# Kernel tuning notes

Hardware: AMD Instinct MI355X
Metric: run time of the kernel (lower is better)

Reference implementation:

```python
import jax, jax.numpy as jnp
import numpy as np

N = 40000   # nodes
E = 150000  # edges (before self-loops)
G = 128     # graphs in batch
V = 20000   # vocab
D = 512     # embedding/hidden dim
H = 4       # heads (layers 0,1)
C = 128     # per-head channels (H*C = D)


def setup_inputs() -> dict:
    key = jax.random.key(0)
    ks = jax.random.split(key, 64)
    n = lambda i, shp, s=0.05: jax.random.normal(ks[i], shp, dtype=jnp.float32) * s
    inp = {}
    inp['node_ids'] = jax.random.randint(ks[0], (N,), 0, V, dtype=jnp.int32)
    inp['edge_index'] = jax.random.randint(ks[1], (2, E), 0, N, dtype=jnp.int32)
    inp['batch'] = jnp.sort(jax.random.randint(ks[2], (N,), 0, G, dtype=jnp.int32))
    inp['emb'] = n(3, (V, D), 0.02)
    # GAT layer 0: D -> H x C, concat
    inp['W0'] = n(4, (D, H * C)); inp['as0'] = n(5, (H, C)); inp['ad0'] = n(6, (H, C)); inp['b0'] = n(7, (D,), 0.01)
    # GAT layer 1: D -> H x C, concat
    inp['W1'] = n(8, (D, H * C)); inp['as1'] = n(9, (H, C)); inp['ad1'] = n(10, (H, C)); inp['b1'] = n(11, (D,), 0.01)
    inp['W2'] = n(12, (D, D)); inp['as2'] = n(13, (1, D)); inp['ad2'] = n(14, (1, D)); inp['b2'] = n(15, (D,), 0.01)
    # danger head
    inp['dW1'] = n(16, (D, D)); inp['db1'] = n(17, (D,), 0.01)
    inp['dg1'] = 1.0 + n(18, (D,), 0.02); inp['dbt1'] = n(19, (D,), 0.02)
    inp['drm1'] = n(20, (D,), 0.02); inp['drv1'] = jax.random.uniform(ks[21], (D,)) + 0.5
    inp['dW2'] = n(22, (D, D // 2)); inp['db2'] = n(23, (D // 2,), 0.01)
    inp['dg2'] = 1.0 + n(24, (D // 2,), 0.02); inp['dbt2'] = n(25, (D // 2,), 0.02)
    inp['drm2'] = n(26, (D // 2,), 0.02); inp['drv2'] = jax.random.uniform(ks[27], (D // 2,)) + 0.5
    inp['dW3'] = n(28, (D // 2, 1)); inp['db3'] = n(29, (1,), 0.01)
    # synergy head
    inp['sW1'] = n(30, (D, D)); inp['sb1'] = n(31, (D,), 0.01)
    inp['sg1'] = 1.0 + n(32, (D,), 0.02); inp['sbt1'] = n(33, (D,), 0.02)
    inp['srm1'] = n(34, (D,), 0.02); inp['srv1'] = jax.random.uniform(ks[35], (D,)) + 0.5
    inp['sW2'] = n(36, (D, D // 2)); inp['sb2'] = n(37, (D // 2,), 0.01)
    inp['sg2'] = 1.0 + n(38, (D // 2,), 0.02); inp['sbt2'] = n(39, (D // 2,), 0.02)
    inp['srm2'] = n(40, (D // 2,), 0.02); inp['srv2'] = jax.random.uniform(ks[41], (D // 2,)) + 0.5
    inp['sW3'] = n(42, (D // 2, 1)); inp['sb3'] = n(43, (1,), 0.01)
    return inp


def _gat(x, W, a_src, a_dst, bias, src, dst, heads, ch, concat):
    # PyG GATConv (eval): linear, per-head additive attention, softmax over
    # incoming edges per destination node, scatter-add aggregate.
    n_nodes = x.shape[0]
    h = (x @ W).reshape(n_nodes, heads, ch)              # [N,H,C]
    e_s = jnp.sum(h * a_src, axis=-1)                    # [N,H]
    e_d = jnp.sum(h * a_dst, axis=-1)                    # [N,H]
    e = jax.nn.leaky_relu(e_s[src] + e_d[dst], 0.2)      # [E,H]
    m = jax.ops.segment_max(e, dst, num_segments=n_nodes)
    m = jnp.where(jnp.isfinite(m), m, 0.0)
    p = jnp.exp(e - m[dst])
    s = jax.ops.segment_sum(p, dst, num_segments=n_nodes)
    alpha = p / (s[dst] + 1e-16)                         # [E,H]
    out = jax.ops.segment_sum(h[src] * alpha[:, :, None], dst, num_segments=n_nodes)
    out = out.reshape(n_nodes, heads * ch) if concat else out.mean(axis=1)
    return out + bias


def _bn(x, g, b, rm, rv):
    return (x - rm) * jax.lax.rsqrt(rv + 1e-5) * g + b


def _head(p, W1, b1, g1, bt1, rm1, rv1, W2, b2, g2, bt2, rm2, rv2, W3, b3):
    z = jax.nn.relu(_bn(p @ W1 + b1, g1, bt1, rm1, rv1))
    z = jax.nn.relu(_bn(z @ W2 + b2, g2, bt2, rm2, rv2))
    return jax.nn.sigmoid(z @ W3 + b3)


def reference(node_ids, edge_index, batch, emb, W0, as0, ad0, b0, W1, as1, ad1, b1, W2, as2, ad2, b2, dW1, db1, dg1, dbt1, drm1, drv1, dW2, db2, dg2, dbt2, drm2, drv2, dW3, db3, sW1, sb1, sg1, sbt1, srm1, srv1, sW2, sb2, sg2, sbt2, srm2, srv2, sW3, sb3):
    loops = jnp.arange(N, dtype=edge_index.dtype)
    src = jnp.concatenate([edge_index[0], loops])
    dst = jnp.concatenate([edge_index[1], loops])
    x = emb[node_ids]                                    # [N,D]
    # layer 0 (no residual)
    x = jax.nn.relu(_gat(x, W0, as0, ad0, b0, src, dst, H, C, True))
    # layer 1 (+residual)
    x = x + jax.nn.relu(_gat(x, W1, as1, ad1, b1, src, dst, H, C, True))
    # layer 2 (+residual)
    x = x + jax.nn.relu(_gat(x, W2, as2, ad2, b2, src, dst, 1, D, False))
    # global mean pool per graph
    sums = jax.ops.segment_sum(x, batch, num_segments=G)
    cnt = jax.ops.segment_sum(jnp.ones((N,), x.dtype), batch, num_segments=G)
    pooled = sums / jnp.maximum(cnt, 1.0)[:, None]       # [G,D]
    danger = _head(pooled, dW1, db1, dg1, dbt1, drm1, drv1, dW2, db2, dg2, dbt2, drm2, drv2, dW3, db3)
    synergy = _head(pooled, sW1, sb1, sg1, sbt1, srm1, srv1, sW2, sb2, sg2, sbt2, srm2, srv2, sW3, sb3)
    return danger, synergy
```

## Files before the change

### kernel.cpp

```cpp
#include <hip/hip_runtime.h>
#include <hip/hip_bf16.h>
#include <stdint.h>

#define NN 40000
#define EE 150000
#define ET 190000
#define GG 128
#define DD 512
#define MP 40064
#define SCAN_B 157
#define PS 16
#define GNB 1252
#define GNBF 1248

typedef __hip_bfloat16 bf16;
typedef __attribute__((ext_vector_type(8))) short s16x8;
typedef __attribute__((ext_vector_type(4))) float f32v4;

__device__ __forceinline__ float b2f(bf16 v) { return __bfloat162float(v); }
__device__ __forceinline__ bf16  f2b(float v) { return __float2bfloat16(v); }
__device__ __forceinline__ unsigned f2bu(float v) {
    bf16 b = __float2bfloat16(v);
    return (unsigned)*(unsigned short*)&b;
}
__device__ __forceinline__ float lo16(unsigned u) { return __uint_as_float(u << 16); }
__device__ __forceinline__ float hi16(unsigned u) { return __uint_as_float(u & 0xffff0000u); }
__device__ __forceinline__ float s2f(short s) {
    return __uint_as_float(((unsigned)(unsigned short)s) << 16);
}

__global__ __launch_bounds__(256) void k_gather_emb(const int* __restrict__ ids,
                                                    const float4* __restrict__ emb4,
                                                    bf16* __restrict__ xb) {
    int t = blockIdx.x * 256 + threadIdx.x;
    int n = t >> 7, c = t & 127;
    if (n >= NN) return;
    int id = ids[n];
    float4 v = emb4[(size_t)id * 128 + c];
    ushort4 u;
    u.x = (unsigned short)f2bu(v.x); u.y = (unsigned short)f2bu(v.y);
    u.z = (unsigned short)f2bu(v.z); u.w = (unsigned short)f2bu(v.w);
    *(ushort4*)(xb + (size_t)n * DD + c * 4) = u;
}

__global__ __launch_bounds__(256) void k_w2bf_t3(const float* __restrict__ W0,
                                                 const float* __restrict__ W1,
                                                 const float* __restrict__ W2,
                                                 bf16* __restrict__ Wt0,
                                                 bf16* __restrict__ Wt1,
                                                 bf16* __restrict__ Wt2) {
    const float* W; bf16* Wt;
    if (blockIdx.z == 0)      { W = W0; Wt = Wt0; }
    else if (blockIdx.z == 1) { W = W1; Wt = Wt1; }
    else                      { W = W2; Wt = Wt2; }
    __shared__ float tile[64][65];
    int tid = threadIdx.x;
    int n0 = blockIdx.x * 64, k0 = blockIdx.y * 64;
    int rr = tid >> 4, cc = (tid & 15) * 4;
    #pragma unroll
    for (int i = 0; i < 4; i++) {
        int k = k0 + i * 16 + rr;
        float4 v = *(const float4*)(W + (size_t)k * DD + n0 + cc);
        tile[cc + 0][i * 16 + rr] = v.x;
        tile[cc + 1][i * 16 + rr] = v.y;
        tile[cc + 2][i * 16 + rr] = v.z;
        tile[cc + 3][i * 16 + rr] = v.w;
    }
    __syncthreads();
    #pragma unroll
    for (int i = 0; i < 4; i++) {
        int nl = i * 16 + rr;
        ushort4 o;
        o.x = (unsigned short)f2bu(tile[nl][cc + 0]);
        o.y = (unsigned short)f2bu(tile[nl][cc + 1]);
        o.z = (unsigned short)f2bu(tile[nl][cc + 2]);
        o.w = (unsigned short)f2bu(tile[nl][cc + 3]);
        *(ushort4*)(Wt + (size_t)(n0 + nl) * DD + k0 + cc) = o;
    }
}

template <int H>
__global__ __launch_bounds__(256) void k_gemm_mfma(const bf16* __restrict__ A,
                                                   const bf16* __restrict__ Bt,
                                                   bf16* __restrict__ C,
                                                   const float* __restrict__ a_s,
                                                   const float* __restrict__ a_d,
                                                   float* __restrict__ es,
                                                   float* __restrict__ ed) {
    constexpr int K = DD, N = DD;
    constexpr int LSTR = 72;
    __shared__ bf16 smem[2 * 128 * LSTR];
    bf16* lA = smem;
    bf16* lB = smem + 128 * LSTR;
    int tid = threadIdx.x, lane = tid & 63, quad = lane >> 4, l16 = lane & 15;
    int w = tid >> 6;

    int bid = blockIdx.x, mt, nt;
    if (bid >= GNBF) { mt = MP / 128 - 1; nt = bid - GNBF; }
    else { nt = (bid & 31) >> 3; mt = (bid >> 5) * 8 + (bid & 7); }
    int m0 = mt * 128, n0 = nt * 128;
    int wm = (w & 1) * 64, wn = (w >> 1) * 64;

    int sdst[4]; const bf16 *pA[4], *pB[4];
    #pragma unroll
    for (int r = 0; r < 4; r++) {
        int q = r * 256 + tid;
        int row = q >> 3, c = q & 7;
        sdst[r] = row * LSTR + c * 8;
        pA[r] = A + (size_t)(m0 + row) * K + c * 8;
        pB[r] = Bt + (size_t)(n0 + row) * K + c * 8;
    }
    int aoff[2][4], boff[2][4];
    #pragma unroll
    for (int kk = 0; kk < 2; kk++)
        #pragma unroll
        for (int i = 0; i < 4; i++) {
            aoff[kk][i] = (wm + i * 16 + l16) * LSTR + (kk * 4 + quad) * 8;
            boff[kk][i] = (wn + i * 16 + l16) * LSTR + (kk * 4 + quad) * 8;
        }

    f32v4 zero = 0;
    f32v4 acc[4][4];
    #pragma unroll
    for (int i = 0; i < 4; i++)
        #pragma unroll
        for (int j = 0; j < 4; j++) acc[i][j] = zero;

    for (int k0 = 0; k0 < K; k0 += 64) {
        __syncthreads();
        #pragma unroll
        for (int r = 0; r < 4; r++) {
            *(s16x8*)(lA + sdst[r]) = *(const s16x8*)(pA[r] + k0);
            *(s16x8*)(lB + sdst[r]) = *(const s16x8*)(pB[r] + k0);
        }
        __syncthreads();
        #pragma unroll
        for (int kk = 0; kk < 2; kk++) {
            s16x8 a[4], b[4];
            #pragma unroll
            for (int i = 0; i < 4; i++) a[i] = *(const s16x8*)(lA + aoff[kk][i]);
            #pragma unroll
            for (int j = 0; j < 4; j++) b[j] = *(const s16x8*)(lB + boff[kk][j]);
            #pragma unroll
            for (int i = 0; i < 4; i++)
                #pragma unroll
                for (int j = 0; j < 4; j++)
                    acc[i][j] = __builtin_amdgcn_mfma_f32_16x16x32_bf16(a[i], b[j], acc[i][j], 0, 0, 0);
        }
    }

    float* asl = (float*)(smem + 8192);
    float* adl = asl + 128;
    __syncthreads();
    if (tid < 128) asl[tid] = a_s[n0 + tid];
    else           adl[tid - 128] = a_d[n0 + tid - 128];

    constexpr int ESTR = 136;
    bf16* ebuf = smem;
    int lrB = (w & 1) * 16 + quad * 4;
    int lr = tid >> 3, cc8 = (tid & 7) * 16;
    int grow = m0 + (lr >> 4) * 64 + (lr & 15);
    int headIdx = (H == 4) ? nt : 0;
    #pragma unroll
    for (int i = 0; i < 4; i++) {
        __syncthreads();
        #pragma unroll
        for (int j = 0; j < 4; j++) {
            int col = wn + j * 16 + l16;
            #pragma unroll
            for (int r = 0; r < 4; r++)
                ebuf[(lrB + r) * ESTR + col] = f2b(acc[i][j][r]);
        }
        __syncthreads();
        s16x8 v0 = *(s16x8*)(ebuf + lr * ESTR + cc8);
        s16x8 v1 = *(s16x8*)(ebuf + lr * ESTR + cc8 + 8);
        float ses = 0.f, sed = 0.f;
        #pragma unroll
        for (int k = 0; k < 8; k++) {
            float x = s2f(v0[k]);
            ses += x * asl[cc8 + k];
            sed += x * adl[cc8 + k];
        }
        #pragma unroll
        for (int k = 0; k < 8; k++) {
            float x = s2f(v1[k]);
            ses += x * asl[cc8 + 8 + k];
            sed += x * adl[cc8 + 8 + k];
        }
        #pragma unroll
        for (int off = 1; off < 8; off <<= 1) {
            ses += __shfl_xor(ses, off, 64);
            sed += __shfl_xor(sed, off, 64);
        }
        int row = grow + i * 16;
        if ((tid & 7) == 0) {
            atomicAdd(es + (size_t)row * H + headIdx, ses);
            atomicAdd(ed + (size_t)row * H + headIdx, sed);
        }
        size_t o = (size_t)row * N + n0 + cc8;
        *(s16x8*)(C + o) = v0;
        *(s16x8*)(C + o + 8) = v1;
    }
}

__global__ __launch_bounds__(256) void k_count_deg(const int* __restrict__ edst,
                                                   int* __restrict__ deg) {
    int e = blockIdx.x * 256 + threadIdx.x;
    if (e >= ET) return;
    int dst = (e < EE) ? edst[e] : (e - EE);
    atomicAdd(&deg[dst], 1);
}

__global__ __launch_bounds__(256) void k_scan_local(const int* __restrict__ deg,
                                                    int* __restrict__ offs,
                                                    int* __restrict__ bsum) {
    __shared__ int buf[256];
    int i = blockIdx.x * 256 + threadIdx.x;
    int v = (i < NN) ? deg[i] : 0;
    buf[threadIdx.x] = v;
    __syncthreads();
    #pragma unroll
    for (int off = 1; off < 256; off <<= 1) {
        int t = (threadIdx.x >= (unsigned)off) ? buf[threadIdx.x - off] : 0;
        __syncthreads();
        buf[threadIdx.x] += t;
        __syncthreads();
    }
    if (i < NN) offs[i] = buf[threadIdx.x] - v;
    if (threadIdx.x == 255) bsum[blockIdx.x] = buf[255];
}

__global__ __launch_bounds__(256) void k_scan_add2(int* __restrict__ offs,
                                                   const int* __restrict__ bsum) {
    __shared__ int buf[256];
    __shared__ int s_off;
    int v = (threadIdx.x < SCAN_B) ? bsum[threadIdx.x] : 0;
    buf[threadIdx.x] = v;
    __syncthreads();
    #pragma unroll
    for (int off = 1; off < 256; off <<= 1) {
        int t = (threadIdx.x >= (unsigned)off) ? buf[threadIdx.x - off] : 0;
        __syncthreads();
        buf[threadIdx.x] += t;
        __syncthreads();
    }
    if (threadIdx.x == blockIdx.x) s_off = buf[threadIdx.x] - v;
    __syncthreads();
    int i = blockIdx.x * 256 + threadIdx.x;
    if (i < NN) offs[i] += s_off;
    if (i == 0) offs[NN] = ET;
}

__global__ __launch_bounds__(256) void k_fill_csr(const int* __restrict__ esrc,
                                                  const int* __restrict__ edst,
                                                  const int* __restrict__ offsets,
                                                  int* __restrict__ cursor,
                                                  int* __restrict__ csr_src) {
    int e = blockIdx.x * 256 + threadIdx.x;
    if (e >= ET) return;
    int dst, src;
    if (e < EE) { dst = edst[e]; src = esrc[e]; }
    else        { dst = e - EE;  src = e - EE; }
    int slot = offsets[dst] + atomicAdd(&cursor[dst], 1);
    csr_src[slot] = src;
}

template <int H, bool RES>
__global__ __launch_bounds__(256) void k_gat_aggregate(const bf16* __restrict__ h,
                                                       const float* __restrict__ es,
                                                       const float* __restrict__ ed,
                                                       const int* __restrict__ offsets,
                                                       const int* __restrict__ csr_src,
                                                       const float* __restrict__ bias,
                                                       bf16* __restrict__ xb) {
    __shared__ int   s_src[8][32];
    __shared__ float s_a[8][32 * H];
    __shared__ int   s_deg[8];
    int tid = threadIdx.x, w = tid >> 6, lane = tid & 63;
    int half = lane >> 5, el = lane & 31;
    int nb = blockIdx.x * 8;
    {
        int ln = w * 2 + half;
        int node = nb + ln;
        int beg = offsets[node];
        int deg = offsets[node + 1] - beg;
        if (deg > 32) deg = 32;
        if (el == 0) s_deg[ln] = deg;
        float edl[H];
        #pragma unroll
        for (int hh = 0; hh < H; hh++) edl[hh] = ed[node * H + hh];
        float e_h[H];
        #pragma unroll
        for (int hh = 0; hh < H; hh++) e_h[hh] = -1e30f;
        if (el < deg) {
            int src = csr_src[beg + el];
            s_src[ln][el] = src;
            if (H == 4) {
                float4 e4 = *(const float4*)(es + (size_t)src * 4);
                float t4[4] = {e4.x, e4.y, e4.z, e4.w};
                #pragma unroll
                for (int hh = 0; hh < 4; hh++) {
                    float e = t4[hh] + edl[hh];
                    e_h[hh] = e > 0.f ? e : 0.2f * e;
                }
            } else {
                float e = es[src] + edl[0];
                e_h[0] = e > 0.f ? e : 0.2f * e;
            }
        }
        float m[H];
        #pragma unroll
        for (int hh = 0; hh < H; hh++) m[hh] = e_h[hh];
        #pragma unroll
        for (int off = 16; off; off >>= 1)
            #pragma unroll
            for (int hh = 0; hh < H; hh++) m[hh] = fmaxf(m[hh], __shfl_xor(m[hh], off, 64));
        float p[H], sum[H];
        #pragma unroll
        for (int hh = 0; hh < H; hh++) {
            p[hh] = (el < deg) ? __expf(e_h[hh] - m[hh]) : 0.f;
            sum[hh] = p[hh];
        }
        #pragma unroll
        for (int off = 16; off; off >>= 1)
            #pragma unroll
            for (int hh = 0; hh < H; hh++) sum[hh] += __shfl_xor(sum[hh], off, 64);
        if (el < deg)
            #pragma unroll
            for (int hh = 0; hh < H; hh++) s_a[ln][el * H + hh] = p[hh] / (sum[hh] + 1e-16f);
    }
    __syncthreads();

    int dbase = lane * 8;
    int hd = (H == 4) ? (lane >> 4) : 0;
    float4 bi0 = *(const float4*)(bias + dbase);
    float4 bi1 = *(const float4*)(bias + dbase + 4);
    #pragma unroll
    for (int t = 0; t < 2; t++) {
        int nn = w * 2 + t;
        int deg = s_deg[nn];
        float acc[8] = {};
        for (int i = 0; i < deg; i++) {
            uint4 u = *(const uint4*)(h + (size_t)s_src[nn][i] * DD + dbase);
            float a = s_a[nn][i * H + hd];
            acc[0] += a * lo16(u.x); acc[1] += a * hi16(u.x);
            acc[2] += a * lo16(u.y); acc[3] += a * hi16(u.y);
            acc[4] += a * lo16(u.z); acc[5] += a * hi16(u.z);
            acc[6] += a * lo16(u.w); acc[7] += a * hi16(u.w);
        }
        float v[8];
        v[0] = acc[0] + bi0.x; v[1] = acc[1] + bi0.y;
        v[2] = acc[2] + bi0.z; v[3] = acc[3] + bi0.w;
        v[4] = acc[4] + bi1.x; v[5] = acc[5] + bi1.y;
        v[6] = acc[6] + bi1.z; v[7] = acc[7] + bi1.w;
        #pragma unroll
        for (int k = 0; k < 8; k++) v[k] = fmaxf(v[k], 0.f);
        size_t base = (size_t)(nb + nn) * DD + dbase;
        if (RES) {
            uint4 u = *(const uint4*)(xb + base);
            v[0] += lo16(u.x); v[1] += hi16(u.x);
            v[2] += lo16(u.y); v[3] += hi16(u.y);
            v[4] += lo16(u.z); v[5] += hi16(u.z);
            v[6] += lo16(u.w); v[7] += hi16(u.w);
        }
        uint4 o;
        o.x = f2bu(v[0]) | (f2bu(v[1]) << 16);
        o.y = f2bu(v[2]) | (f2bu(v[3]) << 16);
        o.z = f2bu(v[4]) | (f2bu(v[5]) << 16);
        o.w = f2bu(v[6]) | (f2bu(v[7]) << 16);
        *(uint4*)(xb + base) = o;
    }
}

__global__ __launch_bounds__(256) void k_pool_part(const int* __restrict__ batch,
                                                   const bf16* __restrict__ xb,
                                                   float* __restrict__ psum,
                                                   int* __restrict__ cnt) {
    int g = blockIdx.x, s = blockIdx.y;
    __shared__ int s_lo, s_hi;
    if (threadIdx.x == 0) {
        int lo = 0, hi = NN;
        while (lo < hi) { int mid = (lo + hi) >> 1; if (batch[mid] < g) lo = mid + 1; else hi = mid; }
        s_lo = lo;
        lo = 0; hi = NN;
        while (lo < hi) { int mid = (lo + hi) >> 1; if (batch[mid] < g + 1) lo = mid + 1; else hi = mid; }
        s_hi = lo;
    }
    __syncthreads();
    int lo = s_lo, hi = s_hi, len = hi - lo;
    int na = lo + (int)(((long)len * s) / PS);
    int nb = lo + (int)(((long)len * (s + 1)) / PS);
    int d0 = threadIdx.x * 2;
    float a0 = 0.f, a1 = 0.f;
    for (int n = na; n < nb; n++) {
        unsigned u = *(const unsigned*)(xb + (size_t)n * DD + d0);
        a0 += lo16(u);
        a1 += hi16(u);
    }
    size_t o = ((size_t)s * GG + g) * DD + d0;
    psum[o]     = a0;
    psum[o + 1] = a1;
    if (s == 0 && threadIdx.x == 0) cnt[g] = len;
}

__global__ __launch_bounds__(256) void k_pool_div(const float* __restrict__ psum,
                                                  const int* __restrict__ cnt,
                                                  float* __restrict__ pooled) {
    int idx = blockIdx.x * 256 + threadIdx.x;
    int g = idx >> 9;
    float s = 0.f;
    #pragma unroll
    for (int seg = 0; seg < PS; seg++) s += psum[(size_t)seg * GG * DD + idx];
    pooled[idx] = s / fmaxf((float)cnt[g], 1.f);
}

template <int Din, int Dout>
__global__ __launch_bounds__(256) void k_head_layer2(const float* __restrict__ inD,
                                                     const float* __restrict__ inS,
                                                     const float* __restrict__ Wd, const float* __restrict__ bd,
                                                     const float* __restrict__ gd, const float* __restrict__ btd,
                                                     const float* __restrict__ rmd, const float* __restrict__ rvd,
                                                     const float* __restrict__ Ws, const float* __restrict__ bs_,
                                                     const float* __restrict__ gs, const float* __restrict__ bts,
                                                     const float* __restrict__ rms, const float* __restrict__ rvs,
                                                     float* __restrict__ outD,
                                                     float* __restrict__ outS) {
    const float *in, *W, *b, *ga, *bt, *rm, *rv; float* out;
    if (blockIdx.z == 0) { in = inD; W = Wd; b = bd; ga = gd; bt = btd; rm = rmd; rv = rvd; out = outD; }
    else                 { in = inS; W = Ws; b = bs_; ga = gs; bt = bts; rm = rms; rv = rvs; out = outS; }
    int g = blockIdx.y;
    int tid = threadIdx.x;
    int j = blockIdx.x * 64 + (tid & 63);
    int ks = tid >> 6;
    __shared__ float s_in[Din];
    __shared__ float s_red[256];
    for (int k = tid; k < Din; k += 256) s_in[k] = in[(size_t)g * Din + k];
    __syncthreads();
    constexpr int KS = Din / 4;
    const float* Wp = W + (size_t)ks * KS * Dout + j;
    float acc = 0.f;
    #pragma unroll 8
    for (int k = 0; k < KS; k++) acc += s_in[ks * KS + k] * Wp[(size_t)k * Dout];
    s_red[tid] = acc;
    __syncthreads();
    if (tid < 64) {
        float s = s_red[tid] + s_red[tid + 64] + s_red[tid + 128] + s_red[tid + 192];
        s += b[j];
        s = (s - rm[j]) * rsqrtf(rv[j] + 1e-5f) * ga[j] + bt[j];
        out[(size_t)g * Dout + j] = s > 0.f ? s : 0.f;
    }
}

__global__ __launch_bounds__(64) void k_head_final2(const float* __restrict__ zD,
                                                    const float* __restrict__ zS,
                                                    const float* __restrict__ W3d, const float* __restrict__ b3d,
                                                    const float* __restrict__ W3s, const float* __restrict__ b3s,
                                                    float* __restrict__ out, int Din) {
    const float* z; const float* W3; const float* b3; float* o;
    if (blockIdx.y == 0) { z = zD; W3 = W3d; b3 = b3d; o = out; }
    else                 { z = zS; W3 = W3s; b3 = b3s; o = out + GG; }
    int g = blockIdx.x, lane = threadIdx.x;
    float s = 0.f;
    for (int k = lane; k < Din; k += 64) s += z[(size_t)g * Din + k] * W3[k];
    #pragma unroll
    for (int off = 32; off; off >>= 1) s += __shfl_xor(s, off, 64);
    if (lane == 0) {
        s += b3[0];
        o[g] = 1.f / (1.f + __expf(-s));
    }
}

extern "C" void kernel_launch(void* const* d_in, const int* in_sizes, int n_in,
                              void* d_out, int out_size, void* d_ws, size_t ws_size,
                              hipStream_t stream) {
    const int*   node_ids = (const int*)d_in[0];
    const int*   ei       = (const int*)d_in[1];
    const int*   batch    = (const int*)d_in[2];
    const float* emb      = (const float*)d_in[3];
    const float* W0  = (const float*)d_in[4],  *as0 = (const float*)d_in[5];
    const float* ad0 = (const float*)d_in[6],  *b0  = (const float*)d_in[7];
    const float* W1  = (const float*)d_in[8],  *as1 = (const float*)d_in[9];
    const float* ad1 = (const float*)d_in[10], *b1  = (const float*)d_in[11];
    const float* W2  = (const float*)d_in[12], *as2 = (const float*)d_in[13];
    const float* ad2 = (const float*)d_in[14], *b2  = (const float*)d_in[15];
    const float* dW1 = (const float*)d_in[16], *db1 = (const float*)d_in[17];
    const float* dg1 = (const float*)d_in[18], *dbt1= (const float*)d_in[19];
    const float* drm1= (const float*)d_in[20], *drv1= (const float*)d_in[21];
    const float* dW2 = (const float*)d_in[22], *db2 = (const float*)d_in[23];
    const float* dg2 = (const float*)d_in[24], *dbt2= (const float*)d_in[25];
    const float* drm2= (const float*)d_in[26], *drv2= (const float*)d_in[27];
    const float* dW3 = (const float*)d_in[28], *db3 = (const float*)d_in[29];
    const float* sW1 = (const float*)d_in[30], *sb1 = (const float*)d_in[31];
    const float* sg1 = (const float*)d_in[32], *sbt1= (const float*)d_in[33];
    const float* srm1= (const float*)d_in[34], *srv1= (const float*)d_in[35];
    const float* sW2 = (const float*)d_in[36], *sb2 = (const float*)d_in[37];
    const float* sg2 = (const float*)d_in[38], *sbt2= (const float*)d_in[39];
    const float* srm2= (const float*)d_in[40], *srv2= (const float*)d_in[41];
    const float* sW3 = (const float*)d_in[42], *sb3 = (const float*)d_in[43];

    const int* esrc = ei;
    const int* edst = ei + EE;

    char* p = (char*)d_ws;
    auto alloc = [&](size_t bytes) { char* r = p; p += (bytes + 255) & ~(size_t)255; return (void*)r; };
    bf16*  xb      = (bf16*)alloc((size_t)MP * DD * 2);
    bf16*  hbuf    = (bf16*)alloc((size_t)MP * DD * 2);
    bf16*  Wt0     = (bf16*)alloc((size_t)DD * DD * 2);
    bf16*  Wt1     = (bf16*)alloc((size_t)DD * DD * 2);
    bf16*  Wt2     = (bf16*)alloc((size_t)DD * DD * 2);
    float* esed    = (float*)alloc((size_t)6 * MP * 4 * 4);
    float* es0 = esed,              *ed0 = esed + (size_t)MP * 4;
    float* es1 = esed + (size_t)MP * 8,  *ed1 = esed + (size_t)MP * 12;
    float* es2 = esed + (size_t)MP * 16, *ed2 = esed + (size_t)MP * 20;
    int*   degcur  = (int*)alloc((size_t)2 * NN * 4);
    int*   deg     = degcur;
    int*   cursor  = degcur + NN;
    int*   offsets = (int*)alloc((size_t)(NN + 1) * 4);
    int*   csr_src = (int*)alloc((size_t)ET * 4);
    int*   bsum    = (int*)alloc((size_t)256 * 4);
    float* psum    = (float*)alloc((size_t)PS * GG * DD * 4);
    int*   cnt     = (int*)alloc((size_t)GG * 4);
    float* pooled  = (float*)alloc((size_t)GG * DD * 4);
    float* z1d     = (float*)alloc((size_t)GG * DD * 4);
    float* z1s     = (float*)alloc((size_t)GG * DD * 4);
    float* z2d     = (float*)alloc((size_t)GG * 256 * 4);
    float* z2s     = (float*)alloc((size_t)GG * 256 * 4);

    hipMemsetAsync(degcur, 0, (size_t)2 * NN * 4, stream);
    hipMemsetAsync(esed, 0, (size_t)6 * MP * 4 * 4, stream);

    k_count_deg<<<(ET + 255) / 256, 256, 0, stream>>>(edst, deg);
    k_scan_local<<<SCAN_B, 256, 0, stream>>>(deg, offsets, bsum);
    k_scan_add2<<<SCAN_B, 256, 0, stream>>>(offsets, bsum);
    k_fill_csr<<<(ET + 255) / 256, 256, 0, stream>>>(esrc, edst, offsets, cursor, csr_src);

    dim3 wgrid(DD / 64, DD / 64, 3);
    k_w2bf_t3<<<wgrid, 256, 0, stream>>>(W0, W1, W2, Wt0, Wt1, Wt2);

    k_gather_emb<<<(NN * 128 + 255) / 256, 256, 0, stream>>>(node_ids, (const float4*)emb, xb);

    k_gemm_mfma<4><<<GNB, 256, 0, stream>>>(xb, Wt0, hbuf, as0, ad0, es0, ed0);
    k_gat_aggregate<4, false><<<NN / 8, 256, 0, stream>>>(hbuf, es0, ed0, offsets, csr_src, b0, xb);

    k_gemm_mfma<4><<<GNB, 256, 0, stream>>>(xb, Wt1, hbuf, as1, ad1, es1, ed1);
    k_gat_aggregate<4, true><<<NN / 8, 256, 0, stream>>>(hbuf, es1, ed1, offsets, csr_src, b1, xb);

    k_gemm_mfma<1><<<GNB, 256, 0, stream>>>(xb, Wt2, hbuf, as2, ad2, es2, ed2);
    k_gat_aggregate<1, true><<<NN / 8, 256, 0, stream>>>(hbuf, es2, ed2, offsets, csr_src, b2, xb);

    dim3 ppgrid(GG, PS);
    k_pool_part<<<ppgrid, 256, 0, stream>>>(batch, xb, psum, cnt);
    k_pool_div<<<(GG * DD) / 256, 256, 0, stream>>>(psum, cnt, pooled);

    float* outp = (float*)d_out;
    dim3 h1grid(DD / 64, GG, 2);
    k_head_layer2<DD, DD><<<h1grid, 256, 0, stream>>>(pooled, pooled,
        dW1, db1, dg1, dbt1, drm1, drv1,
        sW1, sb1, sg1, sbt1, srm1, srv1, z1d, z1s);
    dim3 h2grid(256 / 64, GG, 2);
    k_head_layer2<DD, 256><<<h2grid, 256, 0, stream>>>(z1d, z1s,
        dW2, db2, dg2, dbt2, drm2, drv2,
        sW2, sb2, sg2, sbt2, srm2, srv2, z2d, z2s);
    dim3 fgrid(GG, 2);
    k_head_final2<<<fgrid, 64, 0, stream>>>(z2d, z2s, dW3, db3, sW3, sb3, outp, 256);
}
```

Before: 494.8 us.

## Merge prep kernels, replace attention-logit atomics with plain stores, interleave aggregation

Merges the weight transpose/convert and the embedding gather into one launch. The GEMM epilogue now writes per-tile attention logit partials with plain stores instead of atomics: per head for H=4, and four column-tile partials for H=1 that the aggregate kernel sums. This also lets the memset of the logit buffers be dropped. The aggregation loop now processes the two nodes of each wave in one interleaved loop, giving more independent gathers in flight at the cost of extra registers and per-iteration branches.

```diff
diff --git a/kernel.cpp b/kernel.cpp
--- a/kernel.cpp
+++ b/kernel.cpp
@@ -12,6 +12,7 @@
 #define PS 16
 #define GNB 1252
 #define GNBF 1248
+#define WB 192
 
 typedef __hip_bfloat16 bf16;
 typedef __attribute__((ext_vector_type(8))) short s16x8;
@@ -29,53 +30,55 @@
     return __uint_as_float(((unsigned)(unsigned short)s) << 16);
 }
 
-__global__ __launch_bounds__(256) void k_gather_emb(const int* __restrict__ ids,
-                                                    const float4* __restrict__ emb4,
-                                                    bf16* __restrict__ xb) {
-    int t = blockIdx.x * 256 + threadIdx.x;
-    int n = t >> 7, c = t & 127;
-    if (n >= NN) return;
-    int id = ids[n];
-    float4 v = emb4[(size_t)id * 128 + c];
-    ushort4 u;
-    u.x = (unsigned short)f2bu(v.x); u.y = (unsigned short)f2bu(v.y);
-    u.z = (unsigned short)f2bu(v.z); u.w = (unsigned short)f2bu(v.w);
-    *(ushort4*)(xb + (size_t)n * DD + c * 4) = u;
-}
-
-__global__ __launch_bounds__(256) void k_w2bf_t3(const float* __restrict__ W0,
-                                                 const float* __restrict__ W1,
-                                                 const float* __restrict__ W2,
-                                                 bf16* __restrict__ Wt0,
-                                                 bf16* __restrict__ Wt1,
-                                                 bf16* __restrict__ Wt2) {
-    const float* W; bf16* Wt;
-    if (blockIdx.z == 0)      { W = W0; Wt = Wt0; }
-    else if (blockIdx.z == 1) { W = W1; Wt = Wt1; }
-    else                      { W = W2; Wt = Wt2; }
+__global__ __launch_bounds__(256) void k_prep(const float* __restrict__ W0,
+                                              const float* __restrict__ W1,
+                                              const float* __restrict__ W2,
+                                              bf16* __restrict__ Wt0,
+                                              bf16* __restrict__ Wt1,
+                                              bf16* __restrict__ Wt2,
+                                              const int* __restrict__ ids,
+                                              const float4* __restrict__ emb4,
+                                              bf16* __restrict__ xb) {
     __shared__ float tile[64][65];
-    int tid = threadIdx.x;
-    int n0 = blockIdx.x * 64, k0 = blockIdx.y * 64;
-    int rr = tid >> 4, cc = (tid & 15) * 4;
-    #pragma unroll
-    for (int i = 0; i < 4; i++) {
-        int k = k0 + i * 16 + rr;
-        float4 v = *(const float4*)(W + (size_t)k * DD + n0 + cc);
-        tile[cc + 0][i * 16 + rr] = v.x;
-        tile[cc + 1][i * 16 + rr] = v.y;
-        tile[cc + 2][i * 16 + rr] = v.z;
-        tile[cc + 3][i * 16 + rr] = v.w;
-    }
-    __syncthreads();
-    #pragma unroll
-    for (int i = 0; i < 4; i++) {
-        int nl = i * 16 + rr;
-        ushort4 o;
-        o.x = (unsigned short)f2bu(tile[nl][cc + 0]);
-        o.y = (unsigned short)f2bu(tile[nl][cc + 1]);
-        o.z = (unsigned short)f2bu(tile[nl][cc + 2]);
-        o.w = (unsigned short)f2bu(tile[nl][cc + 3]);
-        *(ushort4*)(Wt + (size_t)(n0 + nl) * DD + k0 + cc) = o;
+    int b = blockIdx.x, tid = threadIdx.x;
+    if (b < WB) {
+        int wi = b >> 6, tl = b & 63;
+        const float* W; bf16* Wt;
+        if (wi == 0)      { W = W0; Wt = Wt0; }
+        else if (wi == 1) { W = W1; Wt = Wt1; }
+        else              { W = W2; Wt = Wt2; }
+        int n0 = (tl & 7) * 64, k0 = (tl >> 3) * 64;
+        int rr = tid >> 4, cc = (tid & 15) * 4;
+        #pragma unroll
+        for (int i = 0; i < 4; i++) {
+            int k = k0 + i * 16 + rr;
+            float4 v = *(const float4*)(W + (size_t)k * DD + n0 + cc);
+            tile[cc + 0][i * 16 + rr] = v.x;
+            tile[cc + 1][i * 16 + rr] = v.y;
+            tile[cc + 2][i * 16 + rr] = v.z;
+            tile[cc + 3][i * 16 + rr] = v.w;
+        }
+        __syncthreads();
+        #pragma unroll
+        for (int i = 0; i < 4; i++) {
+            int nl = i * 16 + rr;
+            ushort4 o;
+            o.x = (unsigned short)f2bu(tile[nl][cc + 0]);
+            o.y = (unsigned short)f2bu(tile[nl][cc + 1]);
+            o.z = (unsigned short)f2bu(tile[nl][cc + 2]);
+            o.w = (unsigned short)f2bu(tile[nl][cc + 3]);
+            *(ushort4*)(Wt + (size_t)(n0 + nl) * DD + k0 + cc) = o;
+        }
+    } else {
+        int t = (b - WB) * 256 + tid;
+        int n = t >> 7, c = t & 127;
+        if (n >= NN) return;
+        int id = ids[n];
+        float4 v = emb4[(size_t)id * 128 + c];
+        ushort4 u;
+        u.x = (unsigned short)f2bu(v.x); u.y = (unsigned short)f2bu(v.y);
+        u.z = (unsigned short)f2bu(v.z); u.w = (unsigned short)f2bu(v.w);
+        *(ushort4*)(xb + (size_t)n * DD + c * 4) = u;
     }
 }
 
@@ -160,7 +163,6 @@
     int lrB = (w & 1) * 16 + quad * 4;
     int lr = tid >> 3, cc8 = (tid & 7) * 16;
     int grow = m0 + (lr >> 4) * 64 + (lr & 15);
-    int headIdx = (H == 4) ? nt : 0;
     #pragma unroll
     for (int i = 0; i < 4; i++) {
         __syncthreads();
@@ -194,8 +196,13 @@
         }
         int row = grow + i * 16;
         if ((tid & 7) == 0) {
-            atomicAdd(es + (size_t)row * H + headIdx, ses);
-            atomicAdd(ed + (size_t)row * H + headIdx, sed);
+            if (H == 4) {
+                es[(size_t)row * 4 + nt] = ses;
+                ed[(size_t)row * 4 + nt] = sed;
+            } else {
+                es[(size_t)nt * MP + row] = ses;
+                ed[(size_t)nt * MP + row] = sed;
+            }
         }
         size_t o = (size_t)row * N + n0 + cc8;
         *(s16x8*)(C + o) = v0;
@@ -287,8 +294,12 @@
         if (deg > 32) deg = 32;
         if (el == 0) s_deg[ln] = deg;
         float edl[H];
-        #pragma unroll
-        for (int hh = 0; hh < H; hh++) edl[hh] = ed[node * H + hh];
+        if (H == 4) {
+            #pragma unroll
+            for (int hh = 0; hh < H; hh++) edl[hh] = ed[node * H + hh];
+        } else {
+            edl[0] = ed[node] + ed[MP + node] + ed[2 * MP + node] + ed[3 * MP + node];
+        }
         float e_h[H];
         #pragma unroll
         for (int hh = 0; hh < H; hh++) e_h[hh] = -1e30f;
@@ -304,7 +315,8 @@
                     e_h[hh] = e > 0.f ? e : 0.2f * e;
                 }
             } else {
-                float e = es[src] + edl[0];
+                float esv = es[src] + es[MP + src] + es[2 * MP + src] + es[3 * MP + src];
+                float e = esv + edl[0];
                 e_h[0] = e > 0.f ? e : 0.2f * e;
             }
         }
@@ -335,24 +347,37 @@
     int hd = (H == 4) ? (lane >> 4) : 0;
     float4 bi0 = *(const float4*)(bias + dbase);
     float4 bi1 = *(const float4*)(bias + dbase + 4);
+    int ln0 = w * 2, ln1 = w * 2 + 1;
+    int deg0 = s_deg[ln0], deg1 = s_deg[ln1];
+    int dmax = deg0 > deg1 ? deg0 : deg1;
+    float A0[8] = {}, A1[8] = {};
+    for (int i = 0; i < dmax; i++) {
+        if (i < deg0) {
+            uint4 u = *(const uint4*)(h + (size_t)s_src[ln0][i] * DD + dbase);
+            float a = s_a[ln0][i * H + hd];
+            A0[0] += a * lo16(u.x); A0[1] += a * hi16(u.x);
+            A0[2] += a * lo16(u.y); A0[3] += a * hi16(u.y);
+            A0[4] += a * lo16(u.z); A0[5] += a * hi16(u.z);
+            A0[6] += a * lo16(u.w); A0[7] += a * hi16(u.w);
+        }
+        if (i < deg1) {
+            uint4 u = *(const uint4*)(h + (size_t)s_src[ln1][i] * DD + dbase);
+            float a = s_a[ln1][i * H + hd];
+            A1[0] += a * lo16(u.x); A1[1] += a * hi16(u.x);
+            A1[2] += a * lo16(u.y); A1[3] += a * hi16(u.y);
+            A1[4] += a * lo16(u.z); A1[5] += a * hi16(u.z);
+            A1[6] += a * lo16(u.w); A1[7] += a * hi16(u.w);
+        }
+    }
     #pragma unroll
     for (int t = 0; t < 2; t++) {
+        float* A = (t == 0) ? A0 : A1;
         int nn = w * 2 + t;
-        int deg = s_deg[nn];
-        float acc[8] = {};
-        for (int i = 0; i < deg; i++) {
-            uint4 u = *(const uint4*)(h + (size_t)s_src[nn][i] * DD + dbase);
-            float a = s_a[nn][i * H + hd];
-            acc[0] += a * lo16(u.x); acc[1] += a * hi16(u.x);
-            acc[2] += a * lo16(u.y); acc[3] += a * hi16(u.y);
-            acc[4] += a * lo16(u.z); acc[5] += a * hi16(u.z);
-            acc[6] += a * lo16(u.w); acc[7] += a * hi16(u.w);
-        }
         float v[8];
-        v[0] = acc[0] + bi0.x; v[1] = acc[1] + bi0.y;
-        v[2] = acc[2] + bi0.z; v[3] = acc[3] + bi0.w;
-        v[4] = acc[4] + bi1.x; v[5] = acc[5] + bi1.y;
-        v[6] = acc[6] + bi1.z; v[7] = acc[7] + bi1.w;
+        v[0] = A[0] + bi0.x; v[1] = A[1] + bi0.y;
+        v[2] = A[2] + bi0.z; v[3] = A[3] + bi0.w;
+        v[4] = A[4] + bi1.x; v[5] = A[5] + bi1.y;
+        v[6] = A[6] + bi1.z; v[7] = A[7] + bi1.w;
         #pragma unroll
         for (int k = 0; k < 8; k++) v[k] = fmaxf(v[k], 0.f);
         size_t base = (size_t)(nb + nn) * DD + dbase;
@@ -527,17 +552,14 @@
     float* z2s     = (float*)alloc((size_t)GG * 256 * 4);
 
     hipMemsetAsync(degcur, 0, (size_t)2 * NN * 4, stream);
-    hipMemsetAsync(esed, 0, (size_t)6 * MP * 4 * 4, stream);
 
     k_count_deg<<<(ET + 255) / 256, 256, 0, stream>>>(edst, deg);
     k_scan_local<<<SCAN_B, 256, 0, stream>>>(deg, offsets, bsum);
     k_scan_add2<<<SCAN_B, 256, 0, stream>>>(offsets, bsum);
     k_fill_csr<<<(ET + 255) / 256, 256, 0, stream>>>(esrc, edst, offsets, cursor, csr_src);
 
-    dim3 wgrid(DD / 64, DD / 64, 3);
-    k_w2bf_t3<<<wgrid, 256, 0, stream>>>(W0, W1, W2, Wt0, Wt1, Wt2);
-
-    k_gather_emb<<<(NN * 128 + 255) / 256, 256, 0, stream>>>(node_ids, (const float4*)emb, xb);
+    k_prep<<<WB + (NN * 128 + 255) / 256, 256, 0, stream>>>(W0, W1, W2, Wt0, Wt1, Wt2,
+                                                            node_ids, (const float4*)emb, xb);
 
     k_gemm_mfma<4><<<GNB, 256, 0, stream>>>(xb, Wt0, hbuf, as0, ad0, es0, ed0);
     k_gat_aggregate<4, false><<<NN / 8, 256, 0, stream>>>(hbuf, es0, ed0, offsets, csr_src, b0, xb);
```

Result: no change. 486.7 us (-1.6%).
